# Optimization experiments

Measured on AMD Instinct MI355X. Metric: run time of the kernel, lower is better.

## Reference

```python
import jax, jax.numpy as jnp
import numpy as np


def setup_inputs() -> dict:
    key = jax.random.key(0)
    ks = jax.random.split(key, 6)
    N, E, F_IN, H, C = 100000, 800000, 96, 128, 64
    x = jax.random.normal(ks[0], (N, F_IN), dtype=jnp.float32)
    W1 = jax.random.normal(ks[1], (F_IN, H), dtype=jnp.float32) * (1.0 / np.sqrt(F_IN))
    b1 = jnp.zeros((H,), dtype=jnp.float32)
    W2 = jax.random.normal(ks[2], (H, C), dtype=jnp.float32) * (1.0 / np.sqrt(H))
    b2 = jnp.zeros((C,), dtype=jnp.float32)
    edge_index = jax.random.randint(ks[3], (2, E), 0, N, dtype=jnp.int64)
    return {"x": x, "W1": W1, "b1": b1, "W2": W2, "b2": b2, "edge_index": edge_index}


def _gcn_norm(edge_index, num_nodes):
    # Add self-loops, compute symmetric normalization D^-1/2 (A+I) D^-1/2.
    loops = jnp.arange(num_nodes, dtype=edge_index.dtype)
    src = jnp.concatenate([edge_index[0], loops])
    dst = jnp.concatenate([edge_index[1], loops])
    deg = jax.ops.segment_sum(jnp.ones_like(dst, dtype=jnp.float32), dst,
                              num_segments=num_nodes)
    dinv = jnp.where(deg > 0, jax.lax.rsqrt(deg), 0.0)
    norm = dinv[src] * dinv[dst]  # [E+N]
    return src, dst, norm


def _gcn_conv(h, W, b, src, dst, norm, num_nodes):
    h = h @ W                              # [N, out] dense GEMM first (PyG order)
    msg = h[src] * norm[:, None]           # gather + scale, [E+N, out]
    agg = jax.ops.segment_sum(msg, dst, num_segments=num_nodes)
    return agg + b


def reference(x, W1, b1, W2, b2, edge_index):
    N = x.shape[0]
    src, dst, norm = _gcn_norm(edge_index, N)
    h = jax.nn.relu(_gcn_conv(x, W1, b1, src, dst, norm, N))
    embedding = h  # post-ReLU, pre-dropout (dropout inactive at eval)
    out = _gcn_conv(h, W2, b2, src, dst, norm, N)
    return jax.nn.log_softmax(out, axis=1), embedding
```

## Files before the change

### kernel.cpp

```cpp
#include <hip/hip_runtime.h>
#include <hip/hip_bf16.h>

#define NN 100000
#define NE 800000
#define FIN 96
#define FH 128
#define FC 64

#define BLOW 9
#define NBK 196
#define BCAP 5120
#define P1E 4096

typedef unsigned short u16;
typedef unsigned int u32;
typedef __attribute__((ext_vector_type(8))) __bf16 bf16x8;
typedef __attribute__((ext_vector_type(4))) float f32x4;

__device__ __forceinline__ float bf2f(u16 u) {
    u32 x = ((u32)u) << 16;
    return __builtin_bit_cast(float, x);
}
__device__ __forceinline__ u16 f2bf(float f) {
    u32 u = __builtin_bit_cast(u32, f);
    u += 0x7fffu + ((u >> 16) & 1u);
    return (u16)(u >> 16);
}
__device__ __forceinline__ void load8f(const u16* p, float* o) {
    uint4 pk = *(const uint4*)p;
    o[0] = bf2f((u16)pk.x); o[1] = bf2f((u16)(pk.x >> 16));
    o[2] = bf2f((u16)pk.y); o[3] = bf2f((u16)(pk.y >> 16));
    o[4] = bf2f((u16)pk.z); o[5] = bf2f((u16)(pk.z >> 16));
    o[6] = bf2f((u16)pk.w); o[7] = bf2f((u16)(pk.w >> 16));
}
__device__ __forceinline__ void store8bf(u16* p, const float* v) {
    uint4 pk;
    pk.x = (u32)f2bf(v[0]) | ((u32)f2bf(v[1]) << 16);
    pk.y = (u32)f2bf(v[2]) | ((u32)f2bf(v[3]) << 16);
    pk.z = (u32)f2bf(v[4]) | ((u32)f2bf(v[5]) << 16);
    pk.w = (u32)f2bf(v[6]) | ((u32)f2bf(v[7]) << 16);
    *(uint4*)p = pk;
}

__global__ __launch_bounds__(256) void k_bin(const int* __restrict__ srcs,
                                             const int* __restrict__ dsts,
                                             int* __restrict__ bucket_cursor,
                                             u32* __restrict__ bucket_data) {
    __shared__ int s_hist[256];
    __shared__ int s_base[256];
    __shared__ int s_cur[256];
    __shared__ int s_gbase[256];
    __shared__ u32 s_sorted[P1E];
    __shared__ unsigned char s_bkt[P1E];
    int t = threadIdx.x;
    int e0 = blockIdx.x * P1E;
    int n = NE - e0; if (n > P1E) n = P1E;
    s_hist[t] = 0;
    __syncthreads();
    u32 rp[16]; int rb[16];
#pragma unroll
    for (int j = 0; j < 16; j++) {
        int i = j * 256 + t;
        rb[j] = -1;
        if (i < n) {
            int s = srcs[e0 + i], d = dsts[e0 + i];
            int b = d >> BLOW;
            rb[j] = b;
            rp[j] = ((u32)(d & ((1 << BLOW) - 1)) << 17) | (u32)s;
            atomicAdd(&s_hist[b], 1);
        }
    }
    __syncthreads();
    int ct = s_hist[t];
    s_base[t] = ct;
    __syncthreads();
    for (int off = 1; off < 256; off <<= 1) {
        int v = (t >= off) ? s_base[t - off] : 0;
        __syncthreads();
        s_base[t] += v;
        __syncthreads();
    }
    int excl = s_base[t] - ct;
    __syncthreads();
    s_base[t] = excl;
    s_cur[t] = excl;
    if (t < NBK) s_gbase[t] = (ct > 0) ? atomicAdd(&bucket_cursor[t], ct) : 0;
    __syncthreads();
#pragma unroll
    for (int j = 0; j < 16; j++) {
        if (rb[j] >= 0) {
            int r = atomicAdd(&s_cur[rb[j]], 1);
            s_sorted[r] = rp[j];
            s_bkt[r] = (unsigned char)rb[j];
        }
    }
    __syncthreads();
    for (int i = t; i < n; i += 256) {
        int b = s_bkt[i];
        int gpos = s_gbase[b] + (i - s_base[b]);
        if (gpos < BCAP)
            bucket_data[(size_t)b * BCAP + gpos] = s_sorted[i];
    }
}

__global__ __launch_bounds__(256) void k_csr(const int* __restrict__ bucket_cursor,
                                             const u32* __restrict__ bucket_data,
                                             int* __restrict__ row_start,
                                             float* __restrict__ dinv,
                                             int* __restrict__ src_sorted) {
    __shared__ int s_c[256];
    __shared__ int s_cnt[512];
    __shared__ int s_ps[256];
    __shared__ int s_off[512];
    __shared__ int s_cur[512];
    __shared__ u32 s_edges[BCAP];
    int t = threadIdx.x;
    int b = blockIdx.x;
    int nbe = bucket_cursor[b];
    if (nbe > BCAP) nbe = BCAP;
    s_c[t] = (t < NBK) ? bucket_cursor[t] : 0;
    __syncthreads();
    for (int off = 1; off < 256; off <<= 1) {
        int v = (t >= off) ? s_c[t - off] : 0;
        __syncthreads();
        s_c[t] += v;
        __syncthreads();
    }
    int bbase = s_c[b] - nbe;
    s_cnt[t] = 0; s_cnt[t + 256] = 0;
    __syncthreads();
    for (int i = t; i < nbe; i += 256) {
        u32 p = bucket_data[(size_t)b * BCAP + i];
        s_edges[i] = p;
        atomicAdd(&s_cnt[p >> 17], 1);
    }
    __syncthreads();
    int c0 = s_cnt[2 * t], c1 = s_cnt[2 * t + 1];
    s_ps[t] = c0 + c1;
    __syncthreads();
    for (int off = 1; off < 256; off <<= 1) {
        int v = (t >= off) ? s_ps[t - off] : 0;
        __syncthreads();
        s_ps[t] += v;
        __syncthreads();
    }
    int pexcl = s_ps[t] - (c0 + c1);
    s_off[2 * t] = pexcl;          s_cur[2 * t] = pexcl;
    s_off[2 * t + 1] = pexcl + c0; s_cur[2 * t + 1] = pexcl + c0;
    __syncthreads();
#pragma unroll
    for (int k = 0; k < 2; k++) {
        int ld = k * 256 + t;
        int gd = b * 512 + ld;
        if (gd < NN) {
            row_start[gd] = bbase + s_off[ld];
            dinv[gd] = rsqrtf((float)s_cnt[ld] + 1.0f);
        }
    }
    if (b == 0 && t == 0) row_start[NN] = NE;
    for (int i = t; i < nbe; i += 256) {
        u32 p = s_edges[i];
        int d = p >> 17;
        int r = atomicAdd(&s_cur[d], 1);
        src_sorted[bbase + r] = (int)(p & 0x1FFFFu);
    }
}

__global__ void k_cvt_x(const float* __restrict__ x, u16* __restrict__ xb) {
    int i = (blockIdx.x * 256 + threadIdx.x) * 4;
    if (i < NN * FIN) {
        float4 f = *(const float4*)(x + i);
        ushort4 o = {f2bf(f.x), f2bf(f.y), f2bf(f.z), f2bf(f.w)};
        *(ushort4*)(xb + i) = o;
    }
}
__global__ void k_cvt_w(const float* __restrict__ W1, const float* __restrict__ W2,
                        u16* __restrict__ W1t, u16* __restrict__ W2t) {
    int i = blockIdx.x * 256 + threadIdx.x;
    if (i < FH * FIN) {
        int n = i / FIN, k = i % FIN;
        W1t[i] = f2bf(W1[k * FH + n]);
    } else if (i < FH * FIN + FC * FH) {
        int j = i - FH * FIN;
        int n = j / FH, k = j % FH;
        W2t[j] = f2bf(W2[k * FC + n]);
    }
}

__global__ void k_agg1(const u16* __restrict__ xb, const float* __restrict__ dinv,
                       const int* __restrict__ row_start, const int* __restrict__ src_sorted,
                       u16* __restrict__ aggx) {
    int tid = blockIdx.x * 256 + threadIdx.x;
    int dst = tid / 12, q = tid % 12;
    if (dst >= NN) return;
    int rs = row_start[dst], re = row_start[dst + 1];
    float dv = dinv[dst];
    float acc[8], v0[8], v1[8];
    load8f(xb + (size_t)dst * FIN + q * 8, acc);
#pragma unroll
    for (int j = 0; j < 8; j++) acc[j] *= dv;
    int e = rs;
    for (; e + 1 < re; e += 2) {
        int s0 = src_sorted[e], s1 = src_sorted[e + 1];
        float d0 = dinv[s0], d1 = dinv[s1];
        load8f(xb + (size_t)s0 * FIN + q * 8, v0);
        load8f(xb + (size_t)s1 * FIN + q * 8, v1);
#pragma unroll
        for (int j = 0; j < 8; j++) acc[j] += v0[j] * d0 + v1[j] * d1;
    }
    if (e < re) {
        int s0 = src_sorted[e];
        float d0 = dinv[s0];
        load8f(xb + (size_t)s0 * FIN + q * 8, v0);
#pragma unroll
        for (int j = 0; j < 8; j++) acc[j] += v0[j] * d0;
    }
#pragma unroll
    for (int j = 0; j < 8; j++) acc[j] *= dv;
    store8bf(aggx + (size_t)dst * FIN + q * 8, acc);
}

#define LDSW 136
__global__ __launch_bounds__(128) void k_gemm12(const u16* __restrict__ aggx,
                                                const u16* __restrict__ W1t,
                                                const float* __restrict__ b1,
                                                const u16* __restrict__ W2t,
                                                float* __restrict__ emb,
                                                u16* __restrict__ zb) {
    __shared__ u16 sh[2][16 * LDSW];
    int wid = threadIdx.x >> 6, lane = threadIdx.x & 63;
    int wave = blockIdx.x * 2 + wid;
    int row0 = wave << 4;
    int m = lane & 15, quad = lane >> 4;
    f32x4 acc[8] = {{0,0,0,0},{0,0,0,0},{0,0,0,0},{0,0,0,0},
                    {0,0,0,0},{0,0,0,0},{0,0,0,0},{0,0,0,0}};
#pragma unroll
    for (int kt = 0; kt < 3; kt++) {
        bf16x8 a = *(const bf16x8*)(const void*)(aggx + (size_t)(row0 + m) * FIN + kt * 32 + quad * 8);
#pragma unroll
        for (int nt = 0; nt < 8; nt++) {
            bf16x8 b = *(const bf16x8*)(const void*)(W1t + (size_t)(nt * 16 + m) * FIN + kt * 32 + quad * 8);
            acc[nt] = __builtin_amdgcn_mfma_f32_16x16x32_bf16(a, b, acc[nt], 0, 0, 0);
        }
    }
    u16* tile = sh[wid];
#pragma unroll
    for (int nt = 0; nt < 8; nt++) {
        int c = nt * 16 + m;
        float bias = b1[c];
#pragma unroll
        for (int i = 0; i < 4; i++) {
            int r = quad * 4 + i;
            float val = acc[nt][i] + bias;
            val = val > 0.0f ? val : 0.0f;
            emb[(size_t)(row0 + r) * FH + c] = val;
            tile[r * LDSW + c] = f2bf(val);
        }
    }
    __syncthreads();
    f32x4 zacc[4] = {{0,0,0,0},{0,0,0,0},{0,0,0,0},{0,0,0,0}};
#pragma unroll
    for (int kt = 0; kt < 4; kt++) {
        bf16x8 a = *(const bf16x8*)(const void*)(tile + m * LDSW + kt * 32 + quad * 8);
#pragma unroll
        for (int nt = 0; nt < 4; nt++) {
            bf16x8 b = *(const bf16x8*)(const void*)(W2t + (size_t)(nt * 16 + m) * FH + kt * 32 + quad * 8);
            zacc[nt] = __builtin_amdgcn_mfma_f32_16x16x32_bf16(a, b, zacc[nt], 0, 0, 0);
        }
    }
#pragma unroll
    for (int nt = 0; nt < 4; nt++) {
        int c = nt * 16 + m;
#pragma unroll
        for (int i = 0; i < 4; i++) {
            int r = row0 + quad * 4 + i;
            zb[(size_t)r * FC + c] = f2bf(zacc[nt][i]);
        }
    }
}

__global__ void k_agg2lsm(const u16* __restrict__ zb, const float* __restrict__ dinv,
                          const int* __restrict__ row_start, const int* __restrict__ src_sorted,
                          const float* __restrict__ b2, float* __restrict__ logits) {
    int wid = threadIdx.x >> 6, lane = threadIdx.x & 63;
    int dst = blockIdx.x * 4 + wid;
    if (dst >= NN) return;
    int rs = row_start[dst], re = row_start[dst + 1];
    float dv = dinv[dst];
    float acc = bf2f(zb[(size_t)dst * FC + lane]) * dv;
    int e = rs;
    for (; e + 1 < re; e += 2) {
        int s0 = src_sorted[e], s1 = src_sorted[e + 1];
        float d0 = dinv[s0], d1 = dinv[s1];
        float v0 = bf2f(zb[(size_t)s0 * FC + lane]);
        float v1 = bf2f(zb[(size_t)s1 * FC + lane]);
        acc += v0 * d0 + v1 * d1;
    }
    if (e < re) {
        int s0 = src_sorted[e];
        acc += bf2f(zb[(size_t)s0 * FC + lane]) * dinv[s0];
    }
    float v = acc * dv + b2[lane];
    float mx = v;
#pragma unroll
    for (int d = 32; d; d >>= 1) mx = fmaxf(mx, __shfl_xor(mx, d, 64));
    float ex = expf(v - mx);
    float s = ex;
#pragma unroll
    for (int d = 32; d; d >>= 1) s += __shfl_xor(s, d, 64);
    logits[(size_t)dst * FC + lane] = v - mx - logf(s);
}

extern "C" void kernel_launch(void* const* d_in, const int* in_sizes, int n_in,
                              void* d_out, int out_size, void* d_ws, size_t ws_size,
                              hipStream_t stream) {
    const float* x  = (const float*)d_in[0];
    const float* W1 = (const float*)d_in[1];
    const float* b1 = (const float*)d_in[2];
    const float* W2 = (const float*)d_in[3];
    const float* b2 = (const float*)d_in[4];
    const int* ei   = (const int*)d_in[5];
    const int* srcs = ei;
    const int* dsts = ei + NE;

    float* logits = (float*)d_out;
    float* emb    = (float*)d_out + (size_t)NN * FC;

    char* w = (char*)d_ws;
    float* dinv       = (float*)w; w += 400000;
    int*   row_start  = (int*)w;   w += 400128;
    int*   src_sorted = (int*)w;   w += 3200000;
    int*   bucket_cursor = (int*)w; w += 1024;
    u16*   xb         = (u16*)w;   w += 19200000;
    u16*   aggx       = (u16*)w;   w += 19200000;
    u16*   W1t        = (u16*)w;   w += 24576;
    u16*   W2t        = (u16*)w;   w += 16384;
    u16*   zb         = (u16*)w;   w += 12800000;
    u32*   bucket_data = (u32*)aggx;

    hipMemsetAsync(bucket_cursor, 0, NBK * 4, stream);
    k_bin<<<(NE + P1E - 1) / P1E, 256, 0, stream>>>(srcs, dsts, bucket_cursor, bucket_data);
    k_csr<<<NBK, 256, 0, stream>>>(bucket_cursor, bucket_data, row_start, dinv, src_sorted);
    k_cvt_x<<<(NN * FIN / 4 + 255) / 256, 256, 0, stream>>>(x, xb);
    k_cvt_w<<<(FH * FIN + FC * FH + 255) / 256, 256, 0, stream>>>(W1, W2, W1t, W2t);
    k_agg1<<<(NN * 12 + 255) / 256, 256, 0, stream>>>(xb, dinv, row_start, src_sorted, aggx);
    k_gemm12<<<NN / 32, 128, 0, stream>>>(aggx, W1t, b1, W2t, emb, zb);
    k_agg2lsm<<<(NN + 3) / 4, 256, 0, stream>>>(zb, dinv, row_start, src_sorted, b2, logits);
}
```

Baseline: 262.7 us.

## Fuse conversion kernels into binning launch and vectorize layer-2 aggregation per 8 lanes

Folds the x and weight bf16 conversion into extra blocks of the edge-binning kernel, which removes two kernel launches and lets the conversion overlap with binning. Layer-2 aggregation now gives each destination 8 threads that each gather 8 bf16 values with 16-byte loads, instead of one wavefront issuing 2-byte loads per lane. The log-softmax reduction moves from a 64-lane shuffle to in-register work plus a 3-step shuffle. The costs are more registers per thread in layer-2 aggregation and a larger block grid for the binning kernel. Note that NBK (196) is the CSR bucket count, while the old k_bin used (NE+P1E-1)/P1E = 196 blocks, so the two values only coincide.

```diff
diff --git a/kernel.cpp b/kernel.cpp
--- a/kernel.cpp
+++ b/kernel.cpp
@@ -11,6 +11,7 @@
 #define NBK 196
 #define BCAP 5120
 #define P1E 4096
+#define NB_CVTX ((NN * FIN / 4 + 255) / 256)
 
 typedef unsigned short u16;
 typedef unsigned int u32;
@@ -42,10 +43,16 @@
     *(uint4*)p = pk;
 }
 
-__global__ __launch_bounds__(256) void k_bin(const int* __restrict__ srcs,
-                                             const int* __restrict__ dsts,
-                                             int* __restrict__ bucket_cursor,
-                                             u32* __restrict__ bucket_data) {
+__global__ __launch_bounds__(256) void k_prep(const int* __restrict__ srcs,
+                                              const int* __restrict__ dsts,
+                                              int* __restrict__ bucket_cursor,
+                                              u32* __restrict__ bucket_data,
+                                              const float* __restrict__ x,
+                                              u16* __restrict__ xb,
+                                              const float* __restrict__ W1,
+                                              const float* __restrict__ W2,
+                                              u16* __restrict__ W1t,
+                                              u16* __restrict__ W2t) {
     __shared__ int s_hist[256];
     __shared__ int s_base[256];
     __shared__ int s_cur[256];
@@ -53,7 +60,31 @@
     __shared__ u32 s_sorted[P1E];
     __shared__ unsigned char s_bkt[P1E];
     int t = threadIdx.x;
-    int e0 = blockIdx.x * P1E;
+    int blk = blockIdx.x;
+    if (blk >= NBK) {
+        int cb = blk - NBK;
+        if (cb < NB_CVTX) {
+            int i = (cb * 256 + t) * 4;
+            if (i < NN * FIN) {
+                float4 f = *(const float4*)(x + i);
+                ushort4 o = {f2bf(f.x), f2bf(f.y), f2bf(f.z), f2bf(f.w)};
+                *(ushort4*)(xb + i) = o;
+            }
+        } else {
+            for (int i = t; i < FH * FIN + FC * FH; i += 256) {
+                if (i < FH * FIN) {
+                    int n = i / FIN, k = i % FIN;
+                    W1t[i] = f2bf(W1[k * FH + n]);
+                } else {
+                    int j = i - FH * FIN;
+                    int n = j / FH, k = j % FH;
+                    W2t[j] = f2bf(W2[k * FC + n]);
+                }
+            }
+        }
+        return;
+    }
+    int e0 = blk * P1E;
     int n = NE - e0; if (n > P1E) n = P1E;
     s_hist[t] = 0;
     __syncthreads();
@@ -166,27 +197,6 @@
     }
 }
 
-__global__ void k_cvt_x(const float* __restrict__ x, u16* __restrict__ xb) {
-    int i = (blockIdx.x * 256 + threadIdx.x) * 4;
-    if (i < NN * FIN) {
-        float4 f = *(const float4*)(x + i);
-        ushort4 o = {f2bf(f.x), f2bf(f.y), f2bf(f.z), f2bf(f.w)};
-        *(ushort4*)(xb + i) = o;
-    }
-}
-__global__ void k_cvt_w(const float* __restrict__ W1, const float* __restrict__ W2,
-                        u16* __restrict__ W1t, u16* __restrict__ W2t) {
-    int i = blockIdx.x * 256 + threadIdx.x;
-    if (i < FH * FIN) {
-        int n = i / FIN, k = i % FIN;
-        W1t[i] = f2bf(W1[k * FH + n]);
-    } else if (i < FH * FIN + FC * FH) {
-        int j = i - FH * FIN;
-        int n = j / FH, k = j % FH;
-        W2t[j] = f2bf(W2[k * FC + n]);
-    }
-}
-
 __global__ void k_agg1(const u16* __restrict__ xb, const float* __restrict__ dinv,
                        const int* __restrict__ row_start, const int* __restrict__ src_sorted,
                        u16* __restrict__ aggx) {
@@ -282,33 +292,48 @@
 __global__ void k_agg2lsm(const u16* __restrict__ zb, const float* __restrict__ dinv,
                           const int* __restrict__ row_start, const int* __restrict__ src_sorted,
                           const float* __restrict__ b2, float* __restrict__ logits) {
-    int wid = threadIdx.x >> 6, lane = threadIdx.x & 63;
-    int dst = blockIdx.x * 4 + wid;
+    int tid = blockIdx.x * 256 + threadIdx.x;
+    int dst = tid >> 3, q = tid & 7;
     if (dst >= NN) return;
     int rs = row_start[dst], re = row_start[dst + 1];
     float dv = dinv[dst];
-    float acc = bf2f(zb[(size_t)dst * FC + lane]) * dv;
+    float acc[8], v0[8], v1[8];
+    load8f(zb + (size_t)dst * FC + q * 8, acc);
+#pragma unroll
+    for (int j = 0; j < 8; j++) acc[j] *= dv;
     int e = rs;
     for (; e + 1 < re; e += 2) {
         int s0 = src_sorted[e], s1 = src_sorted[e + 1];
         float d0 = dinv[s0], d1 = dinv[s1];
-        float v0 = bf2f(zb[(size_t)s0 * FC + lane]);
-        float v1 = bf2f(zb[(size_t)s1 * FC + lane]);
-        acc += v0 * d0 + v1 * d1;
+        load8f(zb + (size_t)s0 * FC + q * 8, v0);
+        load8f(zb + (size_t)s1 * FC + q * 8, v1);
+#pragma unroll
+        for (int j = 0; j < 8; j++) acc[j] += v0[j] * d0 + v1[j] * d1;
     }
     if (e < re) {
         int s0 = src_sorted[e];
-        acc += bf2f(zb[(size_t)s0 * FC + lane]) * dinv[s0];
-    }
-    float v = acc * dv + b2[lane];
-    float mx = v;
-#pragma unroll
-    for (int d = 32; d; d >>= 1) mx = fmaxf(mx, __shfl_xor(mx, d, 64));
-    float ex = expf(v - mx);
-    float s = ex;
-#pragma unroll
-    for (int d = 32; d; d >>= 1) s += __shfl_xor(s, d, 64);
-    logits[(size_t)dst * FC + lane] = v - mx - logf(s);
+        float d0 = dinv[s0];
+        load8f(zb + (size_t)s0 * FC + q * 8, v0);
+#pragma unroll
+        for (int j = 0; j < 8; j++) acc[j] += v0[j] * d0;
+    }
+#pragma unroll
+    for (int j = 0; j < 8; j++) acc[j] = acc[j] * dv + b2[q * 8 + j];
+    float mx = acc[0];
+#pragma unroll
+    for (int j = 1; j < 8; j++) mx = fmaxf(mx, acc[j]);
+#pragma unroll
+    for (int d = 1; d < 8; d <<= 1) mx = fmaxf(mx, __shfl_xor(mx, d, 64));
+    float s = 0.0f;
+#pragma unroll
+    for (int j = 0; j < 8; j++) s += expf(acc[j] - mx);
+#pragma unroll
+    for (int d = 1; d < 8; d <<= 1) s += __shfl_xor(s, d, 64);
+    float lse = mx + logf(s);
+    float4 o0 = {acc[0] - lse, acc[1] - lse, acc[2] - lse, acc[3] - lse};
+    float4 o1 = {acc[4] - lse, acc[5] - lse, acc[6] - lse, acc[7] - lse};
+    *(float4*)(logits + (size_t)dst * FC + q * 8) = o0;
+    *(float4*)(logits + (size_t)dst * FC + q * 8 + 4) = o1;
 }
 
 extern "C" void kernel_launch(void* const* d_in, const int* in_sizes, int n_in,
@@ -339,11 +364,10 @@
     u32*   bucket_data = (u32*)aggx;
 
     hipMemsetAsync(bucket_cursor, 0, NBK * 4, stream);
-    k_bin<<<(NE + P1E - 1) / P1E, 256, 0, stream>>>(srcs, dsts, bucket_cursor, bucket_data);
+    k_prep<<<NBK + NB_CVTX + 1, 256, 0, stream>>>(srcs, dsts, bucket_cursor, bucket_data,
+                                                  x, xb, W1, W2, W1t, W2t);
     k_csr<<<NBK, 256, 0, stream>>>(bucket_cursor, bucket_data, row_start, dinv, src_sorted);
-    k_cvt_x<<<(NN * FIN / 4 + 255) / 256, 256, 0, stream>>>(x, xb);
-    k_cvt_w<<<(FH * FIN + FC * FH + 255) / 256, 256, 0, stream>>>(W1, W2, W1t, W2t);
     k_agg1<<<(NN * 12 + 255) / 256, 256, 0, stream>>>(xb, dinv, row_start, src_sorted, aggx);
     k_gemm12<<<NN / 32, 128, 0, stream>>>(aggx, W1t, b1, W2t, emb, zb);
-    k_agg2lsm<<<(NN + 3) / 4, 256, 0, stream>>>(zb, dinv, row_start, src_sorted, b2, logits);
-}
+    k_agg2lsm<<<(NN * 8 + 255) / 256, 256, 0, stream>>>(zb, dinv, row_start, src_sorted, b2, logits);
+}
```

Measured after the change: 224.7 us. -14.5%, faster.
